# Performance work log

Hardware: AMD Instinct MI355X
Metric: run time of the kernel (lower is better)

Reference implementation:

```python
import jax, jax.numpy as jnp
import numpy as np

K = 2048  # num_embeddings
D = 64    # embedding_dim


def setup_inputs() -> dict:
    key = jax.random.key(0)
    k1, k2 = jax.random.split(key)
    inputs = jax.random.normal(k1, (64, 32, 32, D), dtype=jnp.float32)
    # tf.random_uniform_initializer default: U[0, 1)
    embeddings = jax.random.uniform(k2, (K, D), dtype=jnp.float32)
    return {"inputs": inputs, "embeddings": embeddings}


def reference(inputs, embeddings):
    input_shape = inputs.shape
    flat_inputs = inputs.reshape(-1, D)  # [N, D]
    distances = (
        jnp.sum(flat_inputs ** 2, axis=1, keepdims=True)
        - 2.0 * jnp.matmul(flat_inputs, embeddings.T)
        + jnp.sum(embeddings ** 2, axis=1)
    )
    encoding_indices = jnp.argmin(distances, axis=1)  # [N]
    quantized = embeddings[encoding_indices].reshape(input_shape)
    # straight-through estimator
    quantized = inputs + jax.lax.stop_gradient(quantized - inputs)
    return quantized, encoding_indices, flat_inputs
```

## Files before the change

### kernel.cpp

```cpp
#include <hip/hip_runtime.h>
#include <cfloat>

#define N_TOTAL 65536
#define DIM     64
#define NEMB    2048

typedef __attribute__((ext_vector_type(8))) _Float16 half8;
typedef __attribute__((ext_vector_type(4))) float    floatx4;

__global__ void prep_kernel(const float* __restrict__ emb,
                            half8* __restrict__ ehp, float* __restrict__ en) {
    const int t = blockIdx.x * 256 + threadIdx.x;
    {
        const int l   = t & 63;
        const int ks  = (t >> 6) & 1;
        const int g   = t >> 7;
        const int col = g * 16 + (l & 15);
        const int kb  = ks * 32 + (l >> 4) * 8;
        const float* s = emb + col * DIM + kb;
        float4 v0 = *(const float4*)s, v1 = *(const float4*)(s + 4);
        half8 hv;
        hv[0] = (_Float16)v0.x; hv[1] = (_Float16)v0.y;
        hv[2] = (_Float16)v0.z; hv[3] = (_Float16)v0.w;
        hv[4] = (_Float16)v1.x; hv[5] = (_Float16)v1.y;
        hv[6] = (_Float16)v1.z; hv[7] = (_Float16)v1.w;
        ehp[t] = hv;
    }
    if (t < NEMB * 4) {
        const int row = t >> 2, seg = t & 3;
        const float* s = emb + row * DIM + seg * 16;
        float acc = 0.f;
#pragma unroll
        for (int i = 0; i < 4; ++i) {
            float4 v = ((const float4*)s)[i];
            acc = fmaf(v.x, v.x, acc); acc = fmaf(v.y, v.y, acc);
            acc = fmaf(v.z, v.z, acc); acc = fmaf(v.w, v.w, acc);
        }
        acc += __shfl_xor(acc, 1, 64);
        acc += __shfl_xor(acc, 2, 64);
        if (seg == 0) en[row] = acc;
    }
}

__global__ __launch_bounds__(256, 3) void vq_mfma_kernel(
        const float* __restrict__ x, const float* __restrict__ emb,
        const char* __restrict__ ehb, const float* __restrict__ eng,
        float* __restrict__ quant, float* __restrict__ idxf,
        float* __restrict__ flat) {

    __shared__ uint4 Stage[4][2][256];
    __shared__ float EnS[NEMB];
    __shared__ uint4 Mrg[2][64];

    const int t    = threadIdx.x;
    const int wave = t >> 6, lane = t & 63;
    const int n = lane & 15, q = lane >> 4;
    const int h = wave & 1, p = wave >> 1;
    const int blk0 = blockIdx.x * 64;
    const int row0 = blk0 + p * 32;

    {
        const float4* s4 = (const float4*)(x + (size_t)blk0 * DIM);
        float4*       d4 = (float4*)(flat + (size_t)blk0 * DIM);
#pragma unroll
        for (int i = 0; i < 4; ++i) d4[i * 256 + t] = s4[i * 256 + t];
    }
    {
        const float4* s4 = (const float4*)eng;
        float4*       d4 = (float4*)EnS;
#pragma unroll
        for (int i = 0; i < 2; ++i) d4[i * 256 + t] = s4[i * 256 + t];
    }

    half8 ah[2][2], al[2][2];
#pragma unroll
    for (int tl = 0; tl < 2; ++tl)
#pragma unroll
        for (int ks = 0; ks < 2; ++ks) {
            const float* pp = x + (size_t)(row0 + tl * 16 + n) * DIM + ks * 32 + q * 8;
            float4 v0 = *(const float4*)pp, v1 = *(const float4*)(pp + 4);
            float xv[8] = {v0.x, v0.y, v0.z, v0.w, v1.x, v1.y, v1.z, v1.w};
#pragma unroll
            for (int j = 0; j < 8; ++j) {
                _Float16 hh = (_Float16)xv[j];
                ah[tl][ks][j] = hh;
                al[tl][ks][j] = (_Float16)(xv[j] - (float)hh);
            }
        }

    __syncthreads();

    unsigned best[8], sec[8];
#pragma unroll
    for (int r = 0; r < 8; ++r) { best[r] = 0u; sec[r] = 0u; }

    const char* ebase = ehb + (size_t)h * 131072 + (size_t)lane * 16;

#pragma unroll
    for (int i = 0; i < 4; ++i)
        __builtin_amdgcn_global_load_lds(
            (const __attribute__((address_space(1))) unsigned*)(ebase + i * 1024),
            (__attribute__((address_space(3))) unsigned*)&Stage[wave][0][i * 64],
            16, 0, 0);

#pragma unroll 2
    for (int tile = 0; tile < 32; ++tile) {
        const int buf = tile & 1;
        if (tile < 31) {
            asm volatile("s_waitcnt lgkmcnt(0)" ::: "memory");
            const char* src = ebase + (size_t)(tile + 1) * 4096;
#pragma unroll
            for (int i = 0; i < 4; ++i)
                __builtin_amdgcn_global_load_lds(
                    (const __attribute__((address_space(1))) unsigned*)(src + i * 1024),
                    (__attribute__((address_space(3))) unsigned*)&Stage[wave][buf ^ 1][i * 64],
                    16, 0, 0);
            asm volatile("s_waitcnt vmcnt(4)" ::: "memory");
        } else {
            asm volatile("s_waitcnt vmcnt(0)" ::: "memory");
        }

        half8 b00, b01, b10, b11;
        {
            const __attribute__((address_space(3))) char* sb =
                (const __attribute__((address_space(3))) char*)&Stage[wave][buf][0];
            asm volatile("ds_read_b128 %0, %4\n\t"
                         "ds_read_b128 %1, %4 offset:1024\n\t"
                         "ds_read_b128 %2, %4 offset:2048\n\t"
                         "ds_read_b128 %3, %4 offset:3072\n\t"
                         "s_waitcnt lgkmcnt(0)"
                         : "=&v"(b00), "=&v"(b01), "=&v"(b10), "=&v"(b11)
                         : "v"(sb + lane * 16));
        }

#pragma unroll
        for (int sub = 0; sub < 2; ++sub) {
            const int L = tile * 2 + sub;
            const float env = EnS[h * 1024 + L * 16 + n];
            const float enh = fmaf(-0.5f, env, 128.0f);
            floatx4 a0 = {enh, enh, enh, enh};
            floatx4 a1 = a0;
            half8 bk0 = sub ? b10 : b00;
            half8 bk1 = sub ? b11 : b01;
            a0 = __builtin_amdgcn_mfma_f32_16x16x32_f16(ah[0][0], bk0, a0, 0, 0, 0);
            a0 = __builtin_amdgcn_mfma_f32_16x16x32_f16(al[0][0], bk0, a0, 0, 0, 0);
            a1 = __builtin_amdgcn_mfma_f32_16x16x32_f16(ah[1][0], bk0, a1, 0, 0, 0);
            a1 = __builtin_amdgcn_mfma_f32_16x16x32_f16(al[1][0], bk0, a1, 0, 0, 0);
            a0 = __builtin_amdgcn_mfma_f32_16x16x32_f16(ah[0][1], bk1, a0, 0, 0, 0);
            a0 = __builtin_amdgcn_mfma_f32_16x16x32_f16(al[0][1], bk1, a0, 0, 0, 0);
            a1 = __builtin_amdgcn_mfma_f32_16x16x32_f16(ah[1][1], bk1, a1, 0, 0, 0);
            a1 = __builtin_amdgcn_mfma_f32_16x16x32_f16(al[1][1], bk1, a1, 0, 0, 0);

            const unsigned Lp = (unsigned)(63 - L);
#pragma unroll
            for (int r = 0; r < 8; ++r) {
                float v = (r < 4) ? a0[r] : a1[r - 4];
                unsigned key = (__float_as_uint(v) & 0xFFFFFFC0u) | Lp;
                unsigned lo  = best[r] < key ? best[r] : key;
                best[r] = best[r] > key ? best[r] : key;
                sec[r]  = sec[r] > lo ? sec[r] : lo;
            }
        }
    }

    unsigned bval[8], bcol[8], sval[8], scol[8];
#pragma unroll
    for (int r = 0; r < 8; ++r) {
        bval[r] = best[r] & 0xFFFFFFC0u;
        bcol[r] = (unsigned)(h * 1024 + (63 - (int)(best[r] & 63u)) * 16 + n);
        sval[r] = sec[r] & 0xFFFFFFC0u;
        scol[r] = (unsigned)(h * 1024 + (63 - (int)(sec[r] & 63u)) * 16 + n);
    }
#pragma unroll
    for (int m = 1; m < 16; m <<= 1) {
#pragma unroll
        for (int r = 0; r < 8; ++r) {
            unsigned ov  = (unsigned)__shfl_xor((int)bval[r], m, 64);
            unsigned oc  = (unsigned)__shfl_xor((int)bcol[r], m, 64);
            unsigned ov2 = (unsigned)__shfl_xor((int)sval[r], m, 64);
            unsigned oc2 = (unsigned)__shfl_xor((int)scol[r], m, 64);
            bool ow = (ov > bval[r]) || (ov == bval[r] && oc < bcol[r]);
            unsigned nbv = ow ? ov : bval[r], nbc = ow ? oc : bcol[r];
            unsigned lv  = ow ? bval[r] : ov, lc  = ow ? bcol[r] : oc;
            bool sv2 = (ov2 > sval[r]) || (ov2 == sval[r] && oc2 < scol[r]);
            unsigned bsv = sv2 ? ov2 : sval[r], bsc = sv2 ? oc2 : scol[r];
            bool s3 = (lv > bsv) || (lv == bsv && lc < bsc);
            sval[r] = s3 ? lv : bsv; scol[r] = s3 ? lc : bsc;
            bval[r] = nbv; bcol[r] = nbc;
        }
    }
    if (n == 0) {
#pragma unroll
        for (int r = 0; r < 8; ++r) {
            const int lr = p * 32 + (r >> 2) * 16 + q * 4 + (r & 3);
            Mrg[h][lr] = make_uint4(bval[r], bcol[r], sval[r], scol[r]);
        }
    }
    __syncthreads();

#pragma unroll
    for (int r = 0; r < 4; ++r) {
        const int lr   = wave * 16 + q * 4 + r;
        const int grow = blk0 + lr;
        uint4 c0v = Mrg[0][lr], c1v = Mrg[1][lr];
        int cand[4] = {(int)c0v.y, (int)c0v.w, (int)c1v.y, (int)c1v.w};
        float4 xv = *(const float4*)(x + (size_t)grow * DIM + n * 4);
        float pbest = -FLT_MAX; int cbest = 0;
        float4 ebest = {0.f, 0.f, 0.f, 0.f};
#pragma unroll
        for (int c = 0; c < 4; ++c) {
            float4 e = *(const float4*)(emb + (size_t)cand[c] * DIM + n * 4);
            float pp = (xv.x - 0.5f * e.x) * e.x + (xv.y - 0.5f * e.y) * e.y
                     + (xv.z - 0.5f * e.z) * e.z + (xv.w - 0.5f * e.w) * e.w;
#pragma unroll
            for (int m2 = 1; m2 < 16; m2 <<= 1) pp += __shfl_xor(pp, m2, 64);
            bool take = (pp > pbest) || (pp == pbest && cand[c] < cbest);
            pbest = take ? pp : pbest;
            cbest = take ? cand[c] : cbest;
            ebest.x = take ? e.x : ebest.x; ebest.y = take ? e.y : ebest.y;
            ebest.z = take ? e.z : ebest.z; ebest.w = take ? e.w : ebest.w;
        }
        *(float4*)(quant + (size_t)grow * DIM + n * 4) = ebest;
        if (n == 0) idxf[grow] = (float)cbest;
    }
}

extern "C" void kernel_launch(void* const* d_in, const int* in_sizes, int n_in,
                              void* d_out, int out_size, void* d_ws, size_t ws_size,
                              hipStream_t stream) {
    const float* x   = (const float*)d_in[0];
    const float* emb = (const float*)d_in[1];
    float* out   = (float*)d_out;
    float* quant = out;
    float* idxf  = out + (size_t)N_TOTAL * DIM;
    float* flat  = idxf + N_TOTAL;

    half8* ehp = (half8*)d_ws;
    float* en  = (float*)((char*)d_ws + (size_t)NEMB * DIM * 2);

    prep_kernel<<<64, 256, 0, stream>>>(emb, ehp, en);
    vq_mfma_kernel<<<N_TOTAL / 64, 256, 0, stream>>>(x, emb, (const char*)ehp, en,
                                                     quant, idxf, flat);
}
```

Measured before the change: 128.3 us.

## Load codebook tiles directly into registers instead of staging through LDS

Removes the per-wave LDS staging buffer and async global-to-LDS loads, replacing them with direct global loads into a double-buffered register array, and prefetches the embedding norms from LDS one tile ahead. Launch bounds are raised to 4 blocks per CU, and the MFMA issue order is interleaved so the two accumulator chains alternate. This removes the LDS round trip and explicit waitcnt barriers and cuts LDS use, at the cost of more VGPRs for the register double buffer. The higher occupancy target may cause spills, and leaving load scheduling to the compiler may expose global memory latency.

```diff
diff --git a/kernel.cpp b/kernel.cpp
--- a/kernel.cpp
+++ b/kernel.cpp
@@ -42,13 +42,12 @@
     }
 }
 
-__global__ __launch_bounds__(256, 3) void vq_mfma_kernel(
+__global__ __launch_bounds__(256, 4) void vq_mfma_kernel(
         const float* __restrict__ x, const float* __restrict__ emb,
         const char* __restrict__ ehb, const float* __restrict__ eng,
         float* __restrict__ quant, float* __restrict__ idxf,
         float* __restrict__ flat) {
 
-    __shared__ uint4 Stage[4][2][256];
     __shared__ float EnS[NEMB];
     __shared__ uint4 Mrg[2][64];
 
@@ -96,59 +95,43 @@
 
     const char* ebase = ehb + (size_t)h * 131072 + (size_t)lane * 16;
 
+    half8 bbuf[2][4];
+    float enc[2][2];
 #pragma unroll
     for (int i = 0; i < 4; ++i)
-        __builtin_amdgcn_global_load_lds(
-            (const __attribute__((address_space(1))) unsigned*)(ebase + i * 1024),
-            (__attribute__((address_space(3))) unsigned*)&Stage[wave][0][i * 64],
-            16, 0, 0);
+        bbuf[0][i] = *(const half8*)(ebase + i * 1024);
+#pragma unroll
+    for (int s = 0; s < 2; ++s)
+        enc[0][s] = EnS[h * 1024 + s * 16 + n];
 
 #pragma unroll 2
     for (int tile = 0; tile < 32; ++tile) {
         const int buf = tile & 1;
         if (tile < 31) {
-            asm volatile("s_waitcnt lgkmcnt(0)" ::: "memory");
             const char* src = ebase + (size_t)(tile + 1) * 4096;
 #pragma unroll
             for (int i = 0; i < 4; ++i)
-                __builtin_amdgcn_global_load_lds(
-                    (const __attribute__((address_space(1))) unsigned*)(src + i * 1024),
-                    (__attribute__((address_space(3))) unsigned*)&Stage[wave][buf ^ 1][i * 64],
-                    16, 0, 0);
-            asm volatile("s_waitcnt vmcnt(4)" ::: "memory");
-        } else {
-            asm volatile("s_waitcnt vmcnt(0)" ::: "memory");
-        }
-
-        half8 b00, b01, b10, b11;
-        {
-            const __attribute__((address_space(3))) char* sb =
-                (const __attribute__((address_space(3))) char*)&Stage[wave][buf][0];
-            asm volatile("ds_read_b128 %0, %4\n\t"
-                         "ds_read_b128 %1, %4 offset:1024\n\t"
-                         "ds_read_b128 %2, %4 offset:2048\n\t"
-                         "ds_read_b128 %3, %4 offset:3072\n\t"
-                         "s_waitcnt lgkmcnt(0)"
-                         : "=&v"(b00), "=&v"(b01), "=&v"(b10), "=&v"(b11)
-                         : "v"(sb + lane * 16));
+                bbuf[buf ^ 1][i] = *(const half8*)(src + i * 1024);
+#pragma unroll
+            for (int s = 0; s < 2; ++s)
+                enc[buf ^ 1][s] = EnS[h * 1024 + (tile + 1) * 32 + s * 16 + n];
         }
 
 #pragma unroll
         for (int sub = 0; sub < 2; ++sub) {
             const int L = tile * 2 + sub;
-            const float env = EnS[h * 1024 + L * 16 + n];
-            const float enh = fmaf(-0.5f, env, 128.0f);
+            const float enh = fmaf(-0.5f, enc[buf][sub], 128.0f);
             floatx4 a0 = {enh, enh, enh, enh};
             floatx4 a1 = a0;
-            half8 bk0 = sub ? b10 : b00;
-            half8 bk1 = sub ? b11 : b01;
+            half8 bk0 = bbuf[buf][sub * 2 + 0];
+            half8 bk1 = bbuf[buf][sub * 2 + 1];
             a0 = __builtin_amdgcn_mfma_f32_16x16x32_f16(ah[0][0], bk0, a0, 0, 0, 0);
+            a1 = __builtin_amdgcn_mfma_f32_16x16x32_f16(ah[1][0], bk0, a1, 0, 0, 0);
             a0 = __builtin_amdgcn_mfma_f32_16x16x32_f16(al[0][0], bk0, a0, 0, 0, 0);
-            a1 = __builtin_amdgcn_mfma_f32_16x16x32_f16(ah[1][0], bk0, a1, 0, 0, 0);
             a1 = __builtin_amdgcn_mfma_f32_16x16x32_f16(al[1][0], bk0, a1, 0, 0, 0);
             a0 = __builtin_amdgcn_mfma_f32_16x16x32_f16(ah[0][1], bk1, a0, 0, 0, 0);
+            a1 = __builtin_amdgcn_mfma_f32_16x16x32_f16(ah[1][1], bk1, a1, 0, 0, 0);
             a0 = __builtin_amdgcn_mfma_f32_16x16x32_f16(al[0][1], bk1, a0, 0, 0, 0);
-            a1 = __builtin_amdgcn_mfma_f32_16x16x32_f16(ah[1][1], bk1, a1, 0, 0, 0);
             a1 = __builtin_amdgcn_mfma_f32_16x16x32_f16(al[1][1], bk1, a1, 0, 0, 0);
 
             const unsigned Lp = (unsigned)(63 - L);
```

New measurement: 121.8 us. -5.1%, faster.
